# Optimization experiments

Measured on AMD Instinct MI355X. Metric: run time of the kernel, lower is better.

The kernel has to match this reference:

```python
import jax, jax.numpy as jnp
import numpy as np
import math

B, H, L = 8, 512, 2048
CH = 1          # channels
D2 = 32         # d_state // 2 (conjugate pairs)
DT_MIN, DT_MAX = 0.001, 0.1


def setup_inputs() -> dict:
    key = jax.random.key(0)
    ks = jax.random.split(key, 7)
    u = jax.random.normal(ks[0], (B, H, L), dtype=jnp.float32)
    # Chebyshev initialization (SimpleS4)
    h_scale = jnp.exp(jnp.arange(H, dtype=jnp.float32) / H * math.log(DT_MAX / DT_MIN))
    angles = jnp.arange(D2, dtype=jnp.float32) * jnp.pi
    theta = jnp.broadcast_to(angles[None, None, :], (CH, H, D2)).astype(jnp.float32) + 0.0
    a = -(jnp.broadcast_to(h_scale[None, :, None], (CH, H, D2)).astype(jnp.float32) + 0.0)
    b = jax.random.normal(ks[1], (CH, H, D2), dtype=jnp.float32)
    c = jax.random.normal(ks[2], (CH, H, D2), dtype=jnp.float32)
    x0 = jax.random.normal(ks[3], (CH, H, D2), dtype=jnp.float32)
    D = jax.random.normal(ks[4], (CH, H), dtype=jnp.float32)
    lim = 1.0 / math.sqrt(CH * H)
    W = jax.random.uniform(ks[5], (H, CH * H), minval=-lim, maxval=lim, dtype=jnp.float32)
    bias = jax.random.uniform(ks[6], (H,), minval=-lim, maxval=lim, dtype=jnp.float32)
    return dict(u=u, a=a, theta=theta, b=b, c=c, x0=x0, D=D, W=W, bias=bias)


def fft_conv(u, f):
    # u: (B,H,L), f: (C,H,L) -> causal conv (B,C,H,L) via zero-padded FFT
    n = 2 * u.shape[-1]
    u_f = jnp.fft.rfft(u, n=n)
    f_f = jnp.fft.rfft(f, n=n)
    y = jnp.fft.irfft(jnp.einsum('bhl,chl->bchl', u_f, f_f), n=n)
    return y[..., : u.shape[-1]]


def s4_forward(u, a, theta, b, c, x0, D, W, bias):
    Bsz, Hd, l = u.shape
    T = 1.0 / (l - 1)                                   # quadrature step
    z = T * jnp.arange(l, dtype=u.dtype)                # (L,)
    aa = -jnp.abs(a)                                    # (C,H,D2) stable decay
    # Vandermonde-like basis: exp(a z) cos(theta z), shape (C,H,D2,L)
    base = jnp.exp(aa[..., None] * z) * jnp.cos(theta[..., None] * z)
    q = b * c                                           # (C,H,D2)
    f = 2.0 * T * jnp.einsum('chd,chdl->chl', q, base)  # SSM kernel (C,H,L)
    y = fft_conv(u, f)                                  # (B,C,H,L)
    # trapezoid-rule endpoint correction
    y = y - 0.5 * (jnp.einsum('ch,bhl->bchl', f[:, :, 0], u)
                   + jnp.einsum('chl,bh->bchl', f, u[:, :, 0]))
    # initial-state contribution (x0 term)
    k0 = 2.0 * jnp.einsum('chd,chdl->chl', c * x0, base)
    y = y + k0[None]
    # skip connection D*u
    y = y + jnp.einsum('ch,bhl->bchl', D, u)
    y = y.reshape(Bsz, CH * Hd, l)                      # (B, C*H, L)
    # NonLinear head: GELU -> pointwise Linear(C*H -> H) (transposed conv1x1)
    y = jax.nn.gelu(y, approximate=False)
    out = jnp.einsum('hf,bfl->bhl', W, y) + bias[None, :, None]
    return out


def reference(u, a, theta, b, c, x0, D, W, bias):
    return s4_forward(u, a, theta, b, c, x0, D, W, bias)
```

## Files before the change

### kernel.cpp

```cpp
#include <hip/hip_runtime.h>
#include <hip/hip_bf16.h>

#define B_  8
#define H_  512
#define L_  2048
#define D2_ 32
#define NC_ 64
#define LC_ 32
#define EP  36

typedef __attribute__((ext_vector_type(8))) short short8;
typedef __attribute__((ext_vector_type(8))) _Float16 half8;
typedef __attribute__((ext_vector_type(2))) _Float16 half2v;
typedef __attribute__((ext_vector_type(4))) float float4v;

__device__ __forceinline__ half2v pk_fma16(half2v a, half2v b, half2v c) {
    return __builtin_elementwise_fma(a, b, c);
}

__device__ __forceinline__ float gelu_fast(float x) {
    float q = x * fmaf(0.044715f, x * x, 1.0f);
    float s = __expf(-1.5957691216057308f * q);
    return __fdividef(x, 1.0f + s);
}

__device__ __forceinline__ unsigned pack_bf16x2(float x, float y) {
    __hip_bfloat162 p = __float22bfloat162_rn(make_float2(x, y));
    return *(unsigned*)&p;
}
__device__ __forceinline__ float2 unpack_bf16x2(unsigned v) {
    __hip_bfloat162 p = *(__hip_bfloat162*)&v;
    return __bfloat1622float2(p);
}
__device__ __forceinline__ unsigned pack_f16x2(float x, float y) {
    auto v = __builtin_amdgcn_cvt_pkrtz(x, y);
    return *(unsigned*)&v;
}

__device__ __forceinline__ void load_lds16(const void* g, void* l) {
    __builtin_amdgcn_global_load_lds((const __attribute__((address_space(1))) unsigned int*)g,
                                     (__attribute__((address_space(3))) unsigned int*)l, 16, 0, 0);
}

__global__ __launch_bounds__(256) void fkprep_kernel(
        const float* __restrict__ a, const float* __restrict__ th,
        const float* __restrict__ bb, const float* __restrict__ cc,
        const float* __restrict__ x0, const float* __restrict__ W,
        __hip_bfloat16* __restrict__ Wb, unsigned* __restrict__ FKf,
        _Float16* __restrict__ AB, _Float16* __restrict__ CB,
        _Float16* __restrict__ WPh) {
    __shared__ float avs[32], tvs[32], qds[32], gxs[32], f_lds[32];
    int h = blockIdx.x;
    int t = threadIdx.x;
    const float T = 1.0f / (float)(L_ - 1);
    Wb[(size_t)h * 512 + t]       = __float2bfloat16(W[(size_t)h * 512 + t]);
    Wb[(size_t)h * 512 + t + 256] = __float2bfloat16(W[(size_t)h * 512 + t + 256]);
    if (t < 32) {
        int d = t;
        float av = -fabsf(a[h * D2_ + d]);
        float tv = th[h * D2_ + d];
        avs[d] = av; tvs[d] = tv;
        qds[d] = bb[h * D2_ + d] * cc[h * D2_ + d];
        gxs[d] = 2.0f * cc[h * D2_ + d] * x0[h * D2_ + d];
        #pragma unroll
        for (int k = 0; k < 6; ++k) {
            float len = (float)(32 << k);
            float e2  = __expf(av * T * len);
            float an  = tv * T * len;
            WPh[((size_t)h * 6 + k) * 64 + d]      = (_Float16)(e2 * __cosf(an));
            WPh[((size_t)h * 6 + k) * 64 + 32 + d] = (_Float16)(e2 * __sinf(an));
        }
    }
    __syncthreads();
    int q4 = t & 3, lc = t >> 2;
    float z0 = T * (float)(lc * 32);
    float pr[8], pi[8], wr[8], wi[8], qd[8], gx[8];
    #pragma unroll
    for (int j = 0; j < 8; ++j) {
        int d = q4 * 8 + j;
        float aa = avs[d], tv = tvs[d];
        float e0 = __expf(aa * z0);
        pr[j] = e0 * __cosf(tv * z0);
        pi[j] = e0 * __sinf(tv * z0);
        float e1 = __expf(aa * T);
        wr[j] = e1 * __cosf(tv * T);
        wi[j] = e1 * __sinf(tv * T);
        qd[j] = qds[d];
        gx[j] = gxs[d];
    }
    for (int i = 0; i < 32; ++i) {
        float fa = 0.f, ka = 0.f;
        #pragma unroll
        for (int j = 0; j < 8; ++j) {
            fa = fmaf(qd[j], pr[j], fa);
            ka = fmaf(gx[j], pr[j], ka);
            float nr = fmaf(pr[j], wr[j], -(pi[j] * wi[j]));
            float ni = fmaf(pr[j], wi[j],  (pi[j] * wr[j]));
            pr[j] = nr; pi[j] = ni;
        }
        fa += __shfl_xor(fa, 1); fa += __shfl_xor(fa, 2);
        ka += __shfl_xor(ka, 1); ka += __shfl_xor(ka, 2);
        if (q4 == 0) {
            float fv = 2.0f * T * fa;
            FKf[(size_t)h * L_ + lc * 32 + i] = pack_bf16x2(fv, ka);
            if (lc == 0) f_lds[i] = fv;
        }
    }
    __syncthreads();
    for (int e = t; e < 64 * 32; e += 256) {
        int m = e >> 5, i = e & 31;
        int d = m & 31;
        float av = avs[d], tv = tvs[d];
        float z  = T * (float)(31 - i);
        float ex = __expf(av * z);
        float v  = (m < 32) ? ex * __cosf(tv * z) : ex * __sinf(tv * z);
        AB[(size_t)h * 2048 + e] = (_Float16)v;
    }
    for (int e = t; e < 32 * 96; e += 256) {
        int i = e / 96, k = e - i * 96;
        float v = 0.f;
        if (k < 32) {
            if (k <= i) v = f_lds[i - k];
        } else {
            int d = (k < 64) ? k - 32 : k - 64;
            float av = avs[d], tv = tvs[d];
            float qs = 2.0f * T * qds[d];
            float z  = T * (float)(i + 1);
            float ex = __expf(av * z);
            v = (k < 64) ? qs * ex * __cosf(tv * z) : -qs * ex * __sinf(tv * z);
        }
        CB[(size_t)h * 3072 + e] = (_Float16)v;
    }
}

__global__ __launch_bounds__(128, 8) void scan_mfma_kernel(
        const float* __restrict__ u, const _Float16* __restrict__ AB,
        const _Float16* __restrict__ CB, const unsigned* __restrict__ WPh,
        const float* __restrict__ Dp, const unsigned* __restrict__ FKf,
        __hip_bfloat16* __restrict__ y) {
    __shared__ __align__(16) unsigned El[64 * EP];
    int wid = threadIdx.x >> 6, lane = threadIdx.x & 63;
    int h = blockIdx.x, b = blockIdx.y;
    int ln = lane & 15, qq = lane >> 4;
    const float* ug = u + (size_t)(b * H_ + h) * L_;

    half8 uf[4];
    #pragma unroll
    for (int nb = 0; nb < 4; ++nb) {
        const float* p = ug + (nb * 16 + ln) * 32 + qq * 8;
        float4 a0 = *(const float4*)p;
        float4 a1 = *(const float4*)(p + 4);
        unsigned* vp = (unsigned*)&uf[nb];
        vp[0] = pack_f16x2(a0.x, a0.y);
        vp[1] = pack_f16x2(a0.z, a0.w);
        vp[2] = pack_f16x2(a1.x, a1.y);
        vp[3] = pack_f16x2(a1.z, a1.w);
    }

    const _Float16* ABh = AB + (size_t)h * 2048;
    int j0 = wid * 8 + qq * 2;
    #pragma unroll
    for (int e = 0; e < 2; ++e) {
        half8 af = *(const half8*)&ABh[(e * 32 + wid * 16 + ln) * 32 + qq * 8];
        #pragma unroll
        for (int nb = 0; nb < 4; ++nb) {
            float4v acc = (float4v){0.f, 0.f, 0.f, 0.f};
            acc = __builtin_amdgcn_mfma_f32_16x16x32_f16(af, uf[nb], acc, 0, 0, 0);
            unsigned p0 = pack_f16x2(acc[0], acc[1]);
            unsigned p1 = pack_f16x2(acc[2], acc[3]);
            *(uint2*)&El[(nb * 16 + ln) * EP + e * 16 + j0] = make_uint2(p0, p1);
        }
    }
    asm volatile("s_waitcnt lgkmcnt(0)" ::: "memory");
    __builtin_amdgcn_sched_barrier(0);

    int c = lane;
    unsigned sr[8], si[8];
    {
        const unsigned* rp = &El[c * EP + wid * 8];
        uint4 r0 = *(const uint4*)rp;
        uint4 r1 = *(const uint4*)(rp + 4);
        uint4 i0 = *(const uint4*)(rp + 16);
        uint4 i1 = *(const uint4*)(rp + 20);
        sr[0]=r0.x; sr[1]=r0.y; sr[2]=r0.z; sr[3]=r0.w;
        sr[4]=r1.x; sr[5]=r1.y; sr[6]=r1.z; sr[7]=r1.w;
        si[0]=i0.x; si[1]=i0.y; si[2]=i0.z; si[3]=i0.w;
        si[4]=i1.x; si[5]=i1.y; si[6]=i1.z; si[7]=i1.w;
    }
    const unsigned* mpb = WPh + (size_t)h * 6 * 32;
    #pragma unroll
    for (int st = 0; st < 6; ++st) {
        int off = 1 << st;
        int src = (c - off) & 63;
        bool act = c >= off;
        const unsigned* mp = mpb + st * 32 + wid * 8;
        #pragma unroll
        for (int jj = 0; jj < 8; ++jj) {
            unsigned prp = (unsigned)__shfl((int)sr[jj], src);
            unsigned pip = (unsigned)__shfl((int)si[jj], src);
            if (!act) { prp = 0u; pip = 0u; }
            unsigned mru = mp[jj];
            unsigned miu = mp[16 + jj];
            unsigned min_ = miu ^ 0x80008000u;
            half2v pr = *(half2v*)&prp, pi = *(half2v*)&pip;
            half2v Mr = *(half2v*)&mru, Mi = *(half2v*)&miu, Mni = *(half2v*)&min_;
            half2v s_r = *(half2v*)&sr[jj], s_i = *(half2v*)&si[jj];
            half2v nr = pk_fma16(pr, Mr, pk_fma16(pi, Mni, s_r));
            half2v ni = pk_fma16(pr, Mi, pk_fma16(pi, Mr,  s_i));
            sr[jj] = *(unsigned*)&nr; si[jj] = *(unsigned*)&ni;
        }
    }
    {
        int srcm1 = (c - 1) & 63;
        #pragma unroll
        for (int jj = 0; jj < 8; ++jj) {
            unsigned a0 = (unsigned)__shfl((int)sr[jj], srcm1);
            unsigned b0 = (unsigned)__shfl((int)si[jj], srcm1);
            if (c == 0) { a0 = 0u; b0 = 0u; }
            sr[jj] = a0; si[jj] = b0;
        }
    }
    {
        unsigned* wp = &El[c * EP + wid * 8];
        *(uint4*)wp        = make_uint4(sr[0], sr[1], sr[2], sr[3]);
        *(uint4*)(wp + 4)  = make_uint4(sr[4], sr[5], sr[6], sr[7]);
        *(uint4*)(wp + 16) = make_uint4(si[0], si[1], si[2], si[3]);
        *(uint4*)(wp + 20) = make_uint4(si[4], si[5], si[6], si[7]);
    }
    const unsigned* fgh = FKf + (size_t)h * L_;
    uint4 fkp[2][2];
    #pragma unroll
    for (int nbi = 0; nbi < 2; ++nbi) {
        int col = (2 * wid + nbi) * 16 + ln;
        fkp[nbi][0] = *(const uint4*)&fgh[col * 32 + qq * 4];
        fkp[nbi][1] = *(const uint4*)&fgh[col * 32 + 16 + qq * 4];
    }
    __syncthreads();

    const _Float16* CBh = CB + (size_t)h * 3072;
    float4v acc2[2][2];
    #pragma unroll
    for (int mb = 0; mb < 2; ++mb)
        #pragma unroll
        for (int nbi = 0; nbi < 2; ++nbi)
            acc2[mb][nbi] = (float4v){0.f, 0.f, 0.f, 0.f};
    #pragma unroll
    for (int ks = 0; ks < 3; ++ks) {
        half8 a2[2];
        a2[0] = *(const half8*)&CBh[(ln)      * 96 + ks * 32 + qq * 8];
        a2[1] = *(const half8*)&CBh[(16 + ln) * 96 + ks * 32 + qq * 8];
        #pragma unroll
        for (int nbi = 0; nbi < 2; ++nbi) {
            int col = (2 * wid + nbi) * 16 + ln;
            half8 bfv;
            if (ks == 0) bfv = uf[2 * wid + nbi];
            else {
                int off = (ks == 1) ? 0 : 16;
                bfv = *(const half8*)&El[col * EP + off + qq * 4];
            }
            acc2[0][nbi] = __builtin_amdgcn_mfma_f32_16x16x32_f16(a2[0], bfv, acc2[0][nbi], 0, 0, 0);
            acc2[1][nbi] = __builtin_amdgcn_mfma_f32_16x16x32_f16(a2[1], bfv, acc2[1][nbi], 0, 0, 0);
        }
    }

    float f0; { f0 = unpack_bf16x2(fgh[0]).x; }
    float c0v = Dp[h] - 0.5f * f0;
    float c1v = -0.5f * ug[0];
    #pragma unroll
    for (int nbi = 0; nbi < 2; ++nbi) {
        int col = (2 * wid + nbi) * 16 + ln;
        #pragma unroll
        for (int mb = 0; mb < 2; ++mb) {
            int l0 = col * 32 + mb * 16 + qq * 4;
            float4 u4 = *(const float4*)(ug + l0);
            uint4 fkv = fkp[nbi][mb];
            float us[4] = {u4.x, u4.y, u4.z, u4.w};
            unsigned fs[4] = {fkv.x, fkv.y, fkv.z, fkv.w};
            float g[4];
            #pragma unroll
            for (int r = 0; r < 4; ++r) {
                float2 fk = unpack_bf16x2(fs[r]);
                float yv = acc2[mb][nbi][r] + fmaf(c0v, us[r], fmaf(c1v, fk.x, fk.y));
                g[r] = gelu_fast(yv);
            }
            uint2 yo;
            yo.x = pack_bf16x2(g[0], g[1]);
            yo.y = pack_bf16x2(g[2], g[3]);
            *(uint2*)((short*)y + (size_t)(b * H_ + h) * L_ + l0) = yo;
        }
    }
}

__global__ __launch_bounds__(256) void transpose_y_kernel(
        const __hip_bfloat16* __restrict__ y, __hip_bfloat16* __restrict__ yT) {
    __shared__ short tile[64][72];
    int l0 = blockIdx.x * 64, f0 = blockIdx.y * 64, b = blockIdx.z;
    int t = threadIdx.x;
    int row = t >> 3, col8 = (t & 7) * 8;
    const short* yg = (const short*)y + (size_t)b * H_ * L_;
    #pragma unroll
    for (int r2 = 0; r2 < 64; r2 += 32) {
        int fr = row + r2;
        *(uint4*)&tile[fr][col8 ^ (8 * ((fr >> 3) & 7))] =
            *(const uint4*)&yg[(size_t)(f0 + fr) * L_ + l0 + col8];
    }
    __syncthreads();
    short* og = (short*)yT + (size_t)b * L_ * H_;
    #pragma unroll
    for (int r2 = 0; r2 < 64; r2 += 32) {
        int lrow = row + r2;
        short v[8];
        #pragma unroll
        for (int j = 0; j < 8; ++j) {
            int f = col8 + j;
            v[j] = tile[f][lrow ^ (8 * ((f >> 3) & 7))];
        }
        *(uint4*)&og[(size_t)(l0 + lrow) * H_ + f0 + col8] = *(uint4*)v;
    }
}

__global__ __launch_bounds__(256) void gemm_kernel(
        const __hip_bfloat16* __restrict__ Wb, const __hip_bfloat16* __restrict__ yT,
        const float* __restrict__ bias, float* __restrict__ out) {
    __shared__ __align__(16) short As[64 * 32];
    __shared__ __align__(16) short Bs[128 * 32];
    int l0 = blockIdx.x * 128;
    int h0 = blockIdx.y * 64;
    int b  = blockIdx.z;
    int t    = threadIdx.x;
    int lane = t & 63, wave = t >> 6;
    int m_off = (wave >> 1) * 32, n_off = (wave & 1) * 64;
    int quad = lane >> 4, ln = lane & 15;

    float4v acc[2][4];
    #pragma unroll
    for (int mt = 0; mt < 2; ++mt)
        #pragma unroll
        for (int nt = 0; nt < 4; ++nt)
            acc[mt][nt] = (float4v){0.f, 0.f, 0.f, 0.f};

    const short* Wg = (const short*)Wb;
    const short* Yg = (const short*)(yT + (size_t)b * L_ * H_);

    int r  = t >> 2;
    int qd = t & 3;

    for (int kt = 0; kt < 16; ++kt) {
        int k0 = kt * 32;
        load_lds16(Wg + (h0 + r) * 512 + k0 + qd * 8, &As[t * 8]);
        load_lds16(Yg + (size_t)(l0 + r)      * 512 + k0 + qd * 8, &Bs[t * 8]);
        load_lds16(Yg + (size_t)(l0 + r + 64) * 512 + k0 + qd * 8, &Bs[(t + 256) * 8]);
        __syncthreads();

        short8 af[2], bf[4];
        #pragma unroll
        for (int mt = 0; mt < 2; ++mt)
            af[mt] = *(const short8*)&As[(m_off + mt * 16 + ln) * 32 + quad * 8];
        #pragma unroll
        for (int nt = 0; nt < 4; ++nt)
            bf[nt] = *(const short8*)&Bs[(n_off + nt * 16 + ln) * 32 + quad * 8];
        #pragma unroll
        for (int mt = 0; mt < 2; ++mt)
            #pragma unroll
            for (int nt = 0; nt < 4; ++nt)
                acc[mt][nt] = __builtin_amdgcn_mfma_f32_16x16x32_bf16(
                    af[mt], bf[nt], acc[mt][nt], 0, 0, 0);
        __syncthreads();
    }

    #pragma unroll
    for (int mt = 0; mt < 2; ++mt) {
        #pragma unroll
        for (int nt = 0; nt < 4; ++nt) {
            int hh = h0 + m_off + mt * 16 + quad * 4;
            int ll = l0 + n_off + nt * 16 + ln;
            #pragma unroll
            for (int r2 = 0; r2 < 4; ++r2)
                out[((size_t)(b * H_ + hh + r2)) * L_ + ll] = acc[mt][nt][r2] + bias[hh + r2];
        }
    }
}

extern "C" void kernel_launch(void* const* d_in, const int* in_sizes, int n_in,
                              void* d_out, int out_size, void* d_ws, size_t ws_size,
                              hipStream_t stream) {
    const float* u    = (const float*)d_in[0];
    const float* a    = (const float*)d_in[1];
    const float* th   = (const float*)d_in[2];
    const float* bb   = (const float*)d_in[3];
    const float* cc   = (const float*)d_in[4];
    const float* x0   = (const float*)d_in[5];
    const float* Dp   = (const float*)d_in[6];
    const float* W    = (const float*)d_in[7];
    const float* bias = (const float*)d_in[8];
    float* out = (float*)d_out;
    char* ws = (char*)d_ws;

    unsigned*       FKf = (unsigned*)ws;
    __hip_bfloat16* yT  = (__hip_bfloat16*)(ws + (4ull  << 20));
    __hip_bfloat16* y   = (__hip_bfloat16*)(ws + (20ull << 20));
    __hip_bfloat16* Wb  = (__hip_bfloat16*)(ws + (36ull << 20));
    _Float16*       AB  = (_Float16*)(ws + (37ull << 20));
    _Float16*       CB  = (_Float16*)(ws + (39ull << 20));
    _Float16*       WPh = (_Float16*)(ws + (42ull << 20));

    hipLaunchKernelGGL(fkprep_kernel,     dim3(H_),        dim3(256), 0, stream,
                       a, th, bb, cc, x0, W, Wb, FKf, AB, CB, WPh);
    hipLaunchKernelGGL(scan_mfma_kernel,  dim3(H_, B_),    dim3(128), 0, stream,
                       u, AB, CB, (const unsigned*)WPh, Dp, FKf, y);
    hipLaunchKernelGGL(transpose_y_kernel,dim3(32, 8, 8),  dim3(256), 0, stream, y, yT);
    hipLaunchKernelGGL(gemm_kernel,       dim3(16, 8, 8),  dim3(256), 0, stream,
                       Wb, yT, bias, out);
}
```

Baseline: 169.4 us.

## Fuse y transpose into GEMM B-tile load and drop transpose kernel

Removes the separate transpose kernel and the yT buffer. The GEMM now reads y in its native (feature, length) layout, interleaves pairs of feature rows in registers, and stores them into a swizzled LDS tile for MFMA B operands. The grid is reordered so blocks sharing an l-range run consecutively. It also lowers the scan kernel's min-blocks launch bound from 8 to 6, giving it more register room at the cost of occupancy.

```diff
diff --git a/kernel.cpp b/kernel.cpp
--- a/kernel.cpp
+++ b/kernel.cpp
@@ -133,7 +133,7 @@
     }
 }
 
-__global__ __launch_bounds__(128, 8) void scan_mfma_kernel(
+__global__ __launch_bounds__(128, 6) void scan_mfma_kernel(
         const float* __restrict__ u, const _Float16* __restrict__ AB,
         const _Float16* __restrict__ CB, const unsigned* __restrict__ WPh,
         const float* __restrict__ Dp, const unsigned* __restrict__ FKf,
@@ -291,41 +291,13 @@
     }
 }
 
-__global__ __launch_bounds__(256) void transpose_y_kernel(
-        const __hip_bfloat16* __restrict__ y, __hip_bfloat16* __restrict__ yT) {
-    __shared__ short tile[64][72];
-    int l0 = blockIdx.x * 64, f0 = blockIdx.y * 64, b = blockIdx.z;
-    int t = threadIdx.x;
-    int row = t >> 3, col8 = (t & 7) * 8;
-    const short* yg = (const short*)y + (size_t)b * H_ * L_;
-    #pragma unroll
-    for (int r2 = 0; r2 < 64; r2 += 32) {
-        int fr = row + r2;
-        *(uint4*)&tile[fr][col8 ^ (8 * ((fr >> 3) & 7))] =
-            *(const uint4*)&yg[(size_t)(f0 + fr) * L_ + l0 + col8];
-    }
-    __syncthreads();
-    short* og = (short*)yT + (size_t)b * L_ * H_;
-    #pragma unroll
-    for (int r2 = 0; r2 < 64; r2 += 32) {
-        int lrow = row + r2;
-        short v[8];
-        #pragma unroll
-        for (int j = 0; j < 8; ++j) {
-            int f = col8 + j;
-            v[j] = tile[f][lrow ^ (8 * ((f >> 3) & 7))];
-        }
-        *(uint4*)&og[(size_t)(l0 + lrow) * H_ + f0 + col8] = *(uint4*)v;
-    }
-}
-
 __global__ __launch_bounds__(256) void gemm_kernel(
-        const __hip_bfloat16* __restrict__ Wb, const __hip_bfloat16* __restrict__ yT,
+        const __hip_bfloat16* __restrict__ Wb, const __hip_bfloat16* __restrict__ y,
         const float* __restrict__ bias, float* __restrict__ out) {
-    __shared__ __align__(16) short As[64 * 32];
-    __shared__ __align__(16) short Bs[128 * 32];
-    int l0 = blockIdx.x * 128;
-    int h0 = blockIdx.y * 64;
+    __shared__ __align__(16) short    As[64 * 32];
+    __shared__ __align__(16) unsigned Bs[128 * 16];
+    int h0 = blockIdx.x * 64;
+    int l0 = blockIdx.y * 128;
     int b  = blockIdx.z;
     int t    = threadIdx.x;
     int lane = t & 63, wave = t >> 6;
@@ -340,16 +312,32 @@
             acc[mt][nt] = (float4v){0.f, 0.f, 0.f, 0.f};
 
     const short* Wg = (const short*)Wb;
-    const short* Yg = (const short*)(yT + (size_t)b * L_ * H_);
+    const short* Yg = (const short*)y + (size_t)b * 512 * L_;
 
     int r  = t >> 2;
     int qd = t & 3;
+    int fp = t & 15;
+    int n8 = t >> 4;
 
     for (int kt = 0; kt < 16; ++kt) {
         int k0 = kt * 32;
         load_lds16(Wg + (h0 + r) * 512 + k0 + qd * 8, &As[t * 8]);
-        load_lds16(Yg + (size_t)(l0 + r)      * 512 + k0 + qd * 8, &Bs[t * 8]);
-        load_lds16(Yg + (size_t)(l0 + r + 64) * 512 + k0 + qd * 8, &Bs[(t + 256) * 8]);
+        const short* ypa = Yg + (size_t)(k0 + 2 * fp) * L_ + l0 + n8 * 8;
+        uint4 ya = *(const uint4*)ypa;
+        uint4 yb = *(const uint4*)(ypa + L_);
+        unsigned au[4] = {ya.x, ya.y, ya.z, ya.w};
+        unsigned bu[4] = {yb.x, yb.y, yb.z, yb.w};
+        unsigned pa[8];
+        #pragma unroll
+        for (int i2 = 0; i2 < 4; ++i2) {
+            pa[2 * i2]     = (au[i2] & 0xFFFFu) | (bu[i2] << 16);
+            pa[2 * i2 + 1] = (au[i2] >> 16)     | (bu[i2] & 0xFFFF0000u);
+        }
+        #pragma unroll
+        for (int i = 0; i < 8; ++i) {
+            int n = n8 * 8 + i;
+            Bs[n * 16 + (fp ^ (((n >> 2) & 3) << 2))] = pa[i];
+        }
         __syncthreads();
 
         short8 af[2], bf[4];
@@ -357,8 +345,10 @@
         for (int mt = 0; mt < 2; ++mt)
             af[mt] = *(const short8*)&As[(m_off + mt * 16 + ln) * 32 + quad * 8];
         #pragma unroll
-        for (int nt = 0; nt < 4; ++nt)
-            bf[nt] = *(const short8*)&Bs[(n_off + nt * 16 + ln) * 32 + quad * 8];
+        for (int nt = 0; nt < 4; ++nt) {
+            int n = n_off + nt * 16 + ln;
+            bf[nt] = *(const short8*)&Bs[n * 16 + ((quad * 4) ^ (((n >> 2) & 3) << 2))];
+        }
         #pragma unroll
         for (int mt = 0; mt < 2; ++mt)
             #pragma unroll
@@ -397,7 +387,6 @@
     char* ws = (char*)d_ws;
 
     unsigned*       FKf = (unsigned*)ws;
-    __hip_bfloat16* yT  = (__hip_bfloat16*)(ws + (4ull  << 20));
     __hip_bfloat16* y   = (__hip_bfloat16*)(ws + (20ull << 20));
     __hip_bfloat16* Wb  = (__hip_bfloat16*)(ws + (36ull << 20));
     _Float16*       AB  = (_Float16*)(ws + (37ull << 20));
@@ -408,7 +397,6 @@
                        a, th, bb, cc, x0, W, Wb, FKf, AB, CB, WPh);
     hipLaunchKernelGGL(scan_mfma_kernel,  dim3(H_, B_),    dim3(128), 0, stream,
                        u, AB, CB, (const unsigned*)WPh, Dp, FKf, y);
-    hipLaunchKernelGGL(transpose_y_kernel,dim3(32, 8, 8),  dim3(256), 0, stream, y, yT);
-    hipLaunchKernelGGL(gemm_kernel,       dim3(16, 8, 8),  dim3(256), 0, stream,
-                       Wb, yT, bias, out);
-}
+    hipLaunchKernelGGL(gemm_kernel,       dim3(8, 16, 8),  dim3(256), 0, stream,
+                       Wb, y, bias, out);
+}
```

Measured after the change: 165.7 us. 2.2% less time.
